# Kernel tuning notes

Measured on AMD Instinct MI355X. Metric: run time of the kernel, lower is better.

## Reference

```python
import jax, jax.numpy as jnp
import numpy as np

H1, H2 = 32, 16  # LSTM units per direction (layer 1, layer 2)
F = 64           # input feature dim


def lstm(x, W, U, b, reverse=False, return_sequences=True):
    """Keras-style LSTM. x: [B,T,F]. W:[F,4H], U:[H,4H], b:[4H].
    Gate order i,f,g,o; sigmoid recurrent activation, tanh activation.
    Dropout is inference-mode (identity). If reverse, process time backwards
    (go_backwards=True)."""
    if reverse:
        x = x[:, ::-1]
    B = x.shape[0]
    H = U.shape[0]
    xW = jnp.einsum('btf,fg->btg', x, W) + b  # [B,T,4H] precomputed input gates

    def step(carry, xw_t):
        h, c = carry
        z = xw_t + h @ U                       # [B,4H]
        i, f, g, o = jnp.split(z, 4, axis=-1)
        i = jax.nn.sigmoid(i)
        f = jax.nn.sigmoid(f)
        g = jnp.tanh(g)
        o = jax.nn.sigmoid(o)
        c = f * c + i * g
        h = o * jnp.tanh(c)
        return (h, c), h

    h0 = jnp.zeros((B, H), x.dtype)
    (h_last, _), hs = jax.lax.scan(step, (h0, h0), jnp.swapaxes(xW, 0, 1))
    if return_sequences:
        hs = jnp.swapaxes(hs, 0, 1)  # [B,T,H]
        if reverse:
            hs = hs[:, ::-1]  # Bidirectional re-reverses backward outputs
        return hs
    return h_last


def setup_inputs() -> dict:
    key = jax.random.key(0)
    ks = jax.random.split(key, 17)
    s = 0.05
    d = {
        'inputs': jax.random.normal(ks[0], (4096, 128, F), jnp.float32),
        # layer 1 (bidirectional, 32 units each dir)
        'W1f': jax.random.normal(ks[1], (F, 4 * H1)) * s,
        'U1f': jax.random.normal(ks[2], (H1, 4 * H1)) * s,
        'b1f': jnp.zeros((4 * H1,)),
        'W1b': jax.random.normal(ks[3], (F, 4 * H1)) * s,
        'U1b': jax.random.normal(ks[4], (H1, 4 * H1)) * s,
        'b1b': jnp.zeros((4 * H1,)),
        # layer 2 (bidirectional, 16 units each dir, input 2*H1=64)
        'W2f': jax.random.normal(ks[5], (2 * H1, 4 * H2)) * s,
        'U2f': jax.random.normal(ks[6], (H2, 4 * H2)) * s,
        'b2f': jnp.zeros((4 * H2,)),
        'W2b': jax.random.normal(ks[7], (2 * H1, 4 * H2)) * s,
        'U2b': jax.random.normal(ks[8], (H2, 4 * H2)) * s,
        'b2b': jnp.zeros((4 * H2,)),
        # dense head
        'W3': jax.random.normal(ks[9], (2 * H2, 8)) * s,
        'b3': jnp.zeros((8,)),
        'W4': jax.random.normal(ks[10], (8, 2)) * s,
        'b4': jnp.zeros((2,)),
    }
    return d


def reference(inputs, W1f, U1f, b1f, W1b, U1b, b1b,
              W2f, U2f, b2f, W2b, U2b, b2b, W3, b3, W4, b4):
    # bi_one: concat(forward seq, time-aligned backward seq) -> [B,T,64]
    h1f = lstm(inputs, W1f, U1f, b1f, reverse=False, return_sequences=True)
    h1b = lstm(inputs, W1b, U1b, b1b, reverse=True, return_sequences=True)
    x = jnp.concatenate([h1f, h1b], axis=-1)
    # bi_two: last hidden state of each direction -> [B,32]
    h2f = lstm(x, W2f, U2f, b2f, reverse=False, return_sequences=False)
    h2b = lstm(x, W2b, U2b, b2b, reverse=True, return_sequences=False)
    x = jnp.concatenate([h2f, h2b], axis=-1)
    x = x @ W3 + b3
    x = x * jax.nn.sigmoid(x)  # swish
    x = x @ W4 + b4
    return jax.nn.sigmoid(x)
```

## Files before the change

### kernel.cpp

```cpp
#include <hip/hip_runtime.h>
#include <hip/hip_bf16.h>

#define T 128
#define F 64
#define H1 32
#define G1 128
#define H2 16
#define G2 64

typedef __attribute__((ext_vector_type(8))) short bf16x8;
typedef __attribute__((ext_vector_type(4))) float f32x4;

__device__ __forceinline__ float sigmoidf_(float x) {
    return __builtin_amdgcn_rcpf(1.0f + __expf(-x));
}
__device__ __forceinline__ float tanhf_(float x) {
    return 1.0f - 2.0f * __builtin_amdgcn_rcpf(__expf(2.0f * x) + 1.0f);
}
__device__ __forceinline__ unsigned short f2bf(float f) {
    union { float f; unsigned u; } c; c.f = f;
    unsigned r = c.u + 0x7FFF + ((c.u >> 16) & 1);
    return (unsigned short)(r >> 16);
}
__device__ __forceinline__ void lds_barrier() {
    asm volatile("s_waitcnt lgkmcnt(0)" ::: "memory");
    __builtin_amdgcn_s_barrier();
}

__global__ __launch_bounds__(256) void xcvt(
    const float* __restrict__ x,
    unsigned short* __restrict__ xbf)
{
    __shared__ unsigned short tile[1024];
    const int g  = blockIdx.x;
    const int t0 = blockIdx.y * 8;
    const int m  = threadIdx.x >> 4;
    const int c4 = threadIdx.x & 15;
    const int ks   = c4 >> 3;
    const int quad = (c4 & 7) >> 1;
    const int j0   = (c4 & 1) * 4;
    const int slot = ks * 512 + (m + 16 * quad) * 8 + j0;

    for (int tt = 0; tt < 8; ++tt) {
        const int t = t0 + tt;
        const float4 v = *(const float4*)(x + ((size_t)(g * 16 + m) * T + t) * 64 + c4 * 4);
        ushort4 u;
        u.x = f2bf(v.x); u.y = f2bf(v.y); u.z = f2bf(v.z); u.w = f2bf(v.w);
        *(ushort4*)(tile + slot) = u;
        __syncthreads();
        *(uint2*)(xbf + (size_t)(g * T + t) * 1024 + threadIdx.x * 4) =
            *(const uint2*)(tile + threadIdx.x * 4);
        __syncthreads();
    }
}

__global__ __launch_bounds__(256, 2) void lstm1_fused(
    const unsigned short* __restrict__ xbf,
    const float* __restrict__ W1f, const float* __restrict__ b1f, const float* __restrict__ U1f,
    const float* __restrict__ W1b, const float* __restrict__ b1b, const float* __restrict__ U1b,
    unsigned short* __restrict__ h1)
{
    __shared__ unsigned short hb[2][16 * 40];
    const int tid  = threadIdx.x;
    const int lane = tid & 63;
    const int wv   = __builtin_amdgcn_readfirstlane(tid >> 6);
    const int gh   = wv & 1;
    const int sh   = wv >> 1;
    const int n15  = lane & 15, quad = lane >> 4;
    const int d    = blockIdx.x & 1, g = blockIdx.x >> 1;

    const float* W  = d ? W1b : W1f;
    const float* U  = d ? U1b : U1f;
    const float* bs = d ? b1b : b1f;

    bf16x8 Wf[4][2], Uf[4];
    f32x4 biasC[4];
    #pragma unroll
    for (int i = 0; i < 4; ++i) {
        const int col = (2 * i + gh) * 16 + n15;
        biasC[i] = (f32x4)(bs[col]);
        #pragma unroll
        for (int ks = 0; ks < 2; ++ks) {
            bf16x8 f;
            #pragma unroll
            for (int j = 0; j < 8; ++j)
                f[j] = (short)f2bf(W[(ks * 32 + quad * 8 + j) * G1 + col]);
            Wf[i][ks] = f;
        }
        bf16x8 u;
        #pragma unroll
        for (int j = 0; j < 8; ++j)
            u[j] = (short)f2bf(U[(quad * 8 + j) * G1 + col]);
        Uf[i] = u;
    }

    #pragma unroll
    for (int i = 0; i < 5; ++i) ((unsigned short*)hb)[tid + i * 256] = 0;

    float c0 = 0.0f, c1 = 0.0f;
    const unsigned short* xb = xbf + (size_t)g * T * 1024 + lane * 8;
    unsigned short* h1b0 = h1 + (size_t)g * T * 1024
        + d * 512 + ((quad * 4 + 2 * sh) + 16 * (gh * 2 + (n15 >> 3))) * 8 + (n15 & 7);
    unsigned short* h1b1 = h1b0 + 8;

    f32x4 xaA[4], xaB[4];
    bf16x8 xA0, xA1, xB0, xB1;
    {
        const unsigned short* p0 = xb + (size_t)(d ? (T - 1) : 0) * 1024;
        bf16x8 t0 = *(const bf16x8*)(p0), t1 = *(const bf16x8*)(p0 + 512);
        #pragma unroll
        for (int i = 0; i < 4; ++i) {
            xaA[i] = __builtin_amdgcn_mfma_f32_16x16x32_bf16(t0, Wf[i][0], biasC[i], 0, 0, 0);
            xaA[i] = __builtin_amdgcn_mfma_f32_16x16x32_bf16(t1, Wf[i][1], xaA[i], 0, 0, 0);
        }
        const unsigned short* p1 = xb + (size_t)(d ? (T - 2) : 1) * 1024;
        t0 = *(const bf16x8*)(p1); t1 = *(const bf16x8*)(p1 + 512);
        #pragma unroll
        for (int i = 0; i < 4; ++i) {
            xaB[i] = __builtin_amdgcn_mfma_f32_16x16x32_bf16(t0, Wf[i][0], biasC[i], 0, 0, 0);
            xaB[i] = __builtin_amdgcn_mfma_f32_16x16x32_bf16(t1, Wf[i][1], xaB[i], 0, 0, 0);
        }
        const unsigned short* p2 = xb + (size_t)(d ? (T - 3) : 2) * 1024;
        xA0 = *(const bf16x8*)(p2); xA1 = *(const bf16x8*)(p2 + 512);
        const unsigned short* p3 = xb + (size_t)(d ? (T - 4) : 3) * 1024;
        xB0 = *(const bf16x8*)(p3); xB1 = *(const bf16x8*)(p3 + 512);
    }
    lds_barrier();

    auto step = [&](int s, f32x4* xa, bf16x8& x0, bf16x8& x1) {
        const bf16x8 af = *(const bf16x8*)(hb[s & 1] + n15 * 40 + quad * 8);
        f32x4 a0 = __builtin_amdgcn_mfma_f32_16x16x32_bf16(af, Uf[0], xa[0], 0, 0, 0);
        f32x4 a1 = __builtin_amdgcn_mfma_f32_16x16x32_bf16(af, Uf[1], xa[1], 0, 0, 0);
        f32x4 a2 = __builtin_amdgcn_mfma_f32_16x16x32_bf16(af, Uf[2], xa[2], 0, 0, 0);
        f32x4 a3 = __builtin_amdgcn_mfma_f32_16x16x32_bf16(af, Uf[3], xa[3], 0, 0, 0);

        xa[0] = __builtin_amdgcn_mfma_f32_16x16x32_bf16(x0, Wf[0][0], biasC[0], 0, 0, 0);
        xa[1] = __builtin_amdgcn_mfma_f32_16x16x32_bf16(x0, Wf[1][0], biasC[1], 0, 0, 0);
        xa[2] = __builtin_amdgcn_mfma_f32_16x16x32_bf16(x0, Wf[2][0], biasC[2], 0, 0, 0);
        xa[3] = __builtin_amdgcn_mfma_f32_16x16x32_bf16(x0, Wf[3][0], biasC[3], 0, 0, 0);
        xa[0] = __builtin_amdgcn_mfma_f32_16x16x32_bf16(x1, Wf[0][1], xa[0], 0, 0, 0);
        xa[1] = __builtin_amdgcn_mfma_f32_16x16x32_bf16(x1, Wf[1][1], xa[1], 0, 0, 0);
        xa[2] = __builtin_amdgcn_mfma_f32_16x16x32_bf16(x1, Wf[2][1], xa[2], 0, 0, 0);
        xa[3] = __builtin_amdgcn_mfma_f32_16x16x32_bf16(x1, Wf[3][1], xa[3], 0, 0, 0);

        if (s + 4 < T) {
            const unsigned short* pn = xb + (size_t)(d ? (T - 5 - s) : (s + 4)) * 1024;
            x0 = *(const bf16x8*)(pn); x1 = *(const bf16x8*)(pn + 512);
        }

        const int t = d ? (T - 1 - s) : s;
        float zi0, zi1, zf0, zf1, zg0, zg1, zo0, zo1;
        if (sh == 0) {
            zi0 = a0[0]; zi1 = a0[1]; zf0 = a1[0]; zf1 = a1[1];
            zg0 = a2[0]; zg1 = a2[1]; zo0 = a3[0]; zo1 = a3[1];
        } else {
            zi0 = a0[2]; zi1 = a0[3]; zf0 = a1[2]; zf1 = a1[3];
            zg0 = a2[2]; zg1 = a2[3]; zo0 = a3[2]; zo1 = a3[3];
        }
        {
            const float ig = sigmoidf_(zi0);
            const float fg = sigmoidf_(zf0);
            const float gg = tanhf_(zg0);
            const float og = sigmoidf_(zo0);
            c0 = fg * c0 + ig * gg;
            const float h = og * tanhf_(c0);
            const unsigned short us = f2bf(h);
            hb[(s + 1) & 1][(quad * 4 + 2 * sh) * 40 + gh * 16 + n15] = us;
            h1b0[(size_t)t * 1024] = us;
        }
        {
            const float ig = sigmoidf_(zi1);
            const float fg = sigmoidf_(zf1);
            const float gg = tanhf_(zg1);
            const float og = sigmoidf_(zo1);
            c1 = fg * c1 + ig * gg;
            const float h = og * tanhf_(c1);
            const unsigned short us = f2bf(h);
            hb[(s + 1) & 1][(quad * 4 + 2 * sh + 1) * 40 + gh * 16 + n15] = us;
            h1b1[(size_t)t * 1024] = us;
        }
        lds_barrier();
    };

    #pragma unroll 1
    for (int s = 0; s < T; s += 2) {
        step(s, xaA, xA0, xA1);
        step(s + 1, xaB, xB0, xB1);
    }
}

__global__ __launch_bounds__(512, 2) void lstm2_head(
    const unsigned short* __restrict__ h1,
    const float* __restrict__ W2f, const float* __restrict__ b2f, const float* __restrict__ U2f,
    const float* __restrict__ W2b, const float* __restrict__ b2b, const float* __restrict__ U2b,
    const float* __restrict__ W3, const float* __restrict__ b3,
    const float* __restrict__ W4, const float* __restrict__ b4,
    float* __restrict__ out)
{
    __shared__ unsigned short hb2[2][2][400];
    __shared__ float hfin[2][16][16];
    __shared__ float ybuf[16][9];
    const int tid  = threadIdx.x;
    const int lane = tid & 63;
    const int wv   = __builtin_amdgcn_readfirstlane(tid >> 6);
    const int d    = wv & 1;
    const int sh   = wv >> 1;
    const int n15  = lane & 15, quad = lane >> 4;
    const int g    = blockIdx.x;

    const float* W  = d ? W2b : W2f;
    const float* U  = d ? U2b : U2f;
    const float* bs = d ? b2b : b2f;

    bf16x8 Wf[4][2], Uf[4];
    f32x4 biasC[4];
    #pragma unroll
    for (int i = 0; i < 4; ++i) {
        const int col = i * 16 + n15;
        biasC[i] = (f32x4)(bs[col]);
        #pragma unroll
        for (int ks = 0; ks < 2; ++ks) {
            bf16x8 f;
            #pragma unroll
            for (int j = 0; j < 8; ++j)
                f[j] = (short)f2bf(W[(ks * 32 + quad * 8 + j) * G2 + col]);
            Wf[i][ks] = f;
        }
        bf16x8 u;
        #pragma unroll
        for (int j = 0; j < 8; ++j) {
            const int k = quad * 8 + j;
            u[j] = (k < H2) ? (short)f2bf(U[k * G2 + col]) : (short)0;
        }
        Uf[i] = u;
    }

    #pragma unroll
    for (int i = 0; i < 4; ++i) {
        const int idx = tid + i * 512;
        if (idx < 1600) ((unsigned short*)hb2)[idx] = 0;
    }

    float c = 0.0f, hlast = 0.0f;
    const unsigned short* hl = h1 + (size_t)g * T * 1024 + lane * 8;

    f32x4 xaA[4], xaB[4];
    bf16x8 hA0, hA1, hB0, hB1;
    {
        const unsigned short* p0 = hl + (size_t)(d ? (T - 1) : 0) * 1024;
        bf16x8 t0 = *(const bf16x8*)(p0), t1 = *(const bf16x8*)(p0 + 512);
        #pragma unroll
        for (int i = 0; i < 4; ++i) {
            xaA[i] = __builtin_amdgcn_mfma_f32_16x16x32_bf16(t0, Wf[i][0], biasC[i], 0, 0, 0);
            xaA[i] = __builtin_amdgcn_mfma_f32_16x16x32_bf16(t1, Wf[i][1], xaA[i], 0, 0, 0);
        }
        const unsigned short* p1 = hl + (size_t)(d ? (T - 2) : 1) * 1024;
        t0 = *(const bf16x8*)(p1); t1 = *(const bf16x8*)(p1 + 512);
        #pragma unroll
        for (int i = 0; i < 4; ++i) {
            xaB[i] = __builtin_amdgcn_mfma_f32_16x16x32_bf16(t0, Wf[i][0], biasC[i], 0, 0, 0);
            xaB[i] = __builtin_amdgcn_mfma_f32_16x16x32_bf16(t1, Wf[i][1], xaB[i], 0, 0, 0);
        }
        const unsigned short* p2 = hl + (size_t)(d ? (T - 3) : 2) * 1024;
        hA0 = *(const bf16x8*)(p2); hA1 = *(const bf16x8*)(p2 + 512);
        const unsigned short* p3 = hl + (size_t)(d ? (T - 4) : 3) * 1024;
        hB0 = *(const bf16x8*)(p3); hB1 = *(const bf16x8*)(p3 + 512);
    }
    lds_barrier();

    auto step = [&](int s, f32x4* xa, bf16x8& x0, bf16x8& x1) {
        const bf16x8 af = *(const bf16x8*)(hb2[d][s & 1] + n15 * 24 + quad * 8);
        f32x4 a0 = __builtin_amdgcn_mfma_f32_16x16x32_bf16(af, Uf[0], xa[0], 0, 0, 0);
        f32x4 a1 = __builtin_amdgcn_mfma_f32_16x16x32_bf16(af, Uf[1], xa[1], 0, 0, 0);
        f32x4 a2 = __builtin_amdgcn_mfma_f32_16x16x32_bf16(af, Uf[2], xa[2], 0, 0, 0);
        f32x4 a3 = __builtin_amdgcn_mfma_f32_16x16x32_bf16(af, Uf[3], xa[3], 0, 0, 0);

        xa[0] = __builtin_amdgcn_mfma_f32_16x16x32_bf16(x0, Wf[0][0], biasC[0], 0, 0, 0);
        xa[1] = __builtin_amdgcn_mfma_f32_16x16x32_bf16(x0, Wf[1][0], biasC[1], 0, 0, 0);
        xa[2] = __builtin_amdgcn_mfma_f32_16x16x32_bf16(x0, Wf[2][0], biasC[2], 0, 0, 0);
        xa[3] = __builtin_amdgcn_mfma_f32_16x16x32_bf16(x0, Wf[3][0], biasC[3], 0, 0, 0);
        xa[0] = __builtin_amdgcn_mfma_f32_16x16x32_bf16(x1, Wf[0][1], xa[0], 0, 0, 0);
        xa[1] = __builtin_amdgcn_mfma_f32_16x16x32_bf16(x1, Wf[1][1], xa[1], 0, 0, 0);
        xa[2] = __builtin_amdgcn_mfma_f32_16x16x32_bf16(x1, Wf[2][1], xa[2], 0, 0, 0);
        xa[3] = __builtin_amdgcn_mfma_f32_16x16x32_bf16(x1, Wf[3][1], xa[3], 0, 0, 0);

        if (s + 4 < T) {
            const unsigned short* pn = hl + (size_t)(d ? (T - 5 - s) : (s + 4)) * 1024;
            x0 = *(const bf16x8*)(pn); x1 = *(const bf16x8*)(pn + 512);
        }

        float z0, z1, z2, z3;
        if (sh == 0)      { z0 = a0[0]; z1 = a1[0]; z2 = a2[0]; z3 = a3[0]; }
        else if (sh == 1) { z0 = a0[1]; z1 = a1[1]; z2 = a2[1]; z3 = a3[1]; }
        else if (sh == 2) { z0 = a0[2]; z1 = a1[2]; z2 = a2[2]; z3 = a3[2]; }
        else              { z0 = a0[3]; z1 = a1[3]; z2 = a2[3]; z3 = a3[3]; }
        const float ig = sigmoidf_(z0);
        const float fg = sigmoidf_(z1);
        const float gg = tanhf_(z2);
        const float og = sigmoidf_(z3);
        c = fg * c + ig * gg;
        hlast = og * tanhf_(c);
        hb2[d][(s + 1) & 1][(quad * 4 + sh) * 24 + n15] = f2bf(hlast);
        lds_barrier();
    };

    #pragma unroll 1
    for (int s = 0; s < T; s += 2) {
        step(s, xaA, hA0, hA1);
        step(s + 1, xaB, hB0, hB1);
    }

    hfin[d][quad * 4 + sh][n15] = hlast;
    __syncthreads();

    if (tid < 128) {
        const int s = tid >> 3, u = tid & 7;
        float a = b3[u];
        #pragma unroll
        for (int k = 0; k < H2; ++k) a += hfin[0][s][k] * W3[k * 8 + u];
        #pragma unroll
        for (int k = 0; k < H2; ++k) a += hfin[1][s][k] * W3[(H2 + k) * 8 + u];
        ybuf[s][u] = a * sigmoidf_(a);
    }
    __syncthreads();
    if (tid < 32) {
        const int s = tid >> 1, o = tid & 1;
        float a = b4[o];
        #pragma unroll
        for (int k = 0; k < 8; ++k) a += ybuf[s][k] * W4[k * 2 + o];
        out[(size_t)(g * 16 + s) * 2 + o] = sigmoidf_(a);
    }
}

extern "C" void kernel_launch(void* const* d_in, const int* in_sizes, int n_in,
                              void* d_out, int out_size, void* d_ws, size_t ws_size,
                              hipStream_t stream) {
    const float* x   = (const float*)d_in[0];
    const float* W1f = (const float*)d_in[1];
    const float* U1f = (const float*)d_in[2];
    const float* b1f = (const float*)d_in[3];
    const float* W1b = (const float*)d_in[4];
    const float* U1b = (const float*)d_in[5];
    const float* b1b = (const float*)d_in[6];
    const float* W2f = (const float*)d_in[7];
    const float* U2f = (const float*)d_in[8];
    const float* b2f = (const float*)d_in[9];
    const float* W2b = (const float*)d_in[10];
    const float* U2b = (const float*)d_in[11];
    const float* b2b = (const float*)d_in[12];
    const float* W3  = (const float*)d_in[13];
    const float* b3  = (const float*)d_in[14];
    const float* W4  = (const float*)d_in[15];
    const float* b4  = (const float*)d_in[16];
    float* out = (float*)d_out;

    const int B  = in_sizes[0] / (T * F);
    const int NG = B / 16;

    const size_t perG = (size_t)T * 1024 * sizeof(unsigned short);
    int chG = (int)(ws_size / (2 * perG));
    if (chG > NG) chG = NG;
    if (chG < 1) chG = 1;
    unsigned short* xbf = (unsigned short*)d_ws;
    unsigned short* h1  = xbf + (size_t)chG * T * 1024;

    for (int g0 = 0; g0 < NG; g0 += chG) {
        const int cg = (NG - g0 < chG) ? (NG - g0) : chG;
        dim3 gcv(cg, T / 8);
        xcvt<<<gcv, 256, 0, stream>>>(x + (size_t)g0 * 16 * T * F, xbf);
        lstm1_fused<<<cg * 2, 256, 0, stream>>>(
            xbf, W1f, b1f, U1f, W1b, b1b, U1b, h1);
        lstm2_head<<<cg, 512, 0, stream>>>(
            h1, W2f, b2f, U2f, W2b, b2b, U2b, W3, b3, W4, b4,
            out + (size_t)g0 * 16 * 2);
    }
}
```

Baseline: 383.4 us.

## Split layer-2 LSTM per direction, separate dense head, simplify input conversion

Layer-2 now runs one direction per 256-thread block instead of both directions in one 512-thread block. This doubles the block count and is meant to improve occupancy and parallelism on the serial recurrence. The dense head moves into its own small kernel, which reads final hidden states stored in the xbf workspace. The input bf16 conversion becomes a one-float4-per-thread scatter with no LDS staging or barriers, at the cost of less coalesced stores and one extra kernel launch per chunk.

```diff
diff --git a/kernel.cpp b/kernel.cpp
--- a/kernel.cpp
+++ b/kernel.cpp
@@ -11,6 +11,8 @@
 typedef __attribute__((ext_vector_type(8))) short bf16x8;
 typedef __attribute__((ext_vector_type(4))) float f32x4;
 
+#define MFMA __builtin_amdgcn_mfma_f32_16x16x32_bf16
+
 __device__ __forceinline__ float sigmoidf_(float x) {
     return __builtin_amdgcn_rcpf(1.0f + __expf(-x));
 }
@@ -31,27 +33,21 @@
     const float* __restrict__ x,
     unsigned short* __restrict__ xbf)
 {
-    __shared__ unsigned short tile[1024];
-    const int g  = blockIdx.x;
-    const int t0 = blockIdx.y * 8;
-    const int m  = threadIdx.x >> 4;
-    const int c4 = threadIdx.x & 15;
-    const int ks   = c4 >> 3;
-    const int quad = (c4 & 7) >> 1;
-    const int j0   = (c4 & 1) * 4;
-    const int slot = ks * 512 + (m + 16 * quad) * 8 + j0;
-
-    for (int tt = 0; tt < 8; ++tt) {
-        const int t = t0 + tt;
-        const float4 v = *(const float4*)(x + ((size_t)(g * 16 + m) * T + t) * 64 + c4 * 4);
-        ushort4 u;
-        u.x = f2bf(v.x); u.y = f2bf(v.y); u.z = f2bf(v.z); u.w = f2bf(v.w);
-        *(ushort4*)(tile + slot) = u;
-        __syncthreads();
-        *(uint2*)(xbf + (size_t)(g * T + t) * 1024 + threadIdx.x * 4) =
-            *(const uint2*)(tile + threadIdx.x * 4);
-        __syncthreads();
-    }
+    const size_t fi = (size_t)blockIdx.x * 256 + threadIdx.x;
+    const int c4 = (int)(fi & 15);
+    const size_t row = fi >> 4;
+    const int t = (int)(row & (T - 1));
+    const size_t b = row >> 7;
+    const int m = (int)(b & 15);
+    const size_t g = b >> 4;
+
+    const float4 v = *(const float4*)(x + fi * 4);
+    ushort4 u;
+    u.x = f2bf(v.x); u.y = f2bf(v.y); u.z = f2bf(v.z); u.w = f2bf(v.w);
+    const int ks = c4 >> 3;
+    const int q  = (c4 & 7) >> 1;
+    const int j0 = (c4 & 1) * 4;
+    *(ushort4*)(xbf + ((size_t)(g * T + t)) * 1024 + ks * 512 + (m + 16 * q) * 8 + j0) = u;
 }
 
 __global__ __launch_bounds__(256, 2) void lstm1_fused(
@@ -110,15 +106,15 @@
         bf16x8 t0 = *(const bf16x8*)(p0), t1 = *(const bf16x8*)(p0 + 512);
         #pragma unroll
         for (int i = 0; i < 4; ++i) {
-            xaA[i] = __builtin_amdgcn_mfma_f32_16x16x32_bf16(t0, Wf[i][0], biasC[i], 0, 0, 0);
-            xaA[i] = __builtin_amdgcn_mfma_f32_16x16x32_bf16(t1, Wf[i][1], xaA[i], 0, 0, 0);
+            xaA[i] = MFMA(t0, Wf[i][0], biasC[i], 0, 0, 0);
+            xaA[i] = MFMA(t1, Wf[i][1], xaA[i], 0, 0, 0);
         }
         const unsigned short* p1 = xb + (size_t)(d ? (T - 2) : 1) * 1024;
         t0 = *(const bf16x8*)(p1); t1 = *(const bf16x8*)(p1 + 512);
         #pragma unroll
         for (int i = 0; i < 4; ++i) {
-            xaB[i] = __builtin_amdgcn_mfma_f32_16x16x32_bf16(t0, Wf[i][0], biasC[i], 0, 0, 0);
-            xaB[i] = __builtin_amdgcn_mfma_f32_16x16x32_bf16(t1, Wf[i][1], xaB[i], 0, 0, 0);
+            xaB[i] = MFMA(t0, Wf[i][0], biasC[i], 0, 0, 0);
+            xaB[i] = MFMA(t1, Wf[i][1], xaB[i], 0, 0, 0);
         }
         const unsigned short* p2 = xb + (size_t)(d ? (T - 3) : 2) * 1024;
         xA0 = *(const bf16x8*)(p2); xA1 = *(const bf16x8*)(p2 + 512);
@@ -129,19 +125,19 @@
 
     auto step = [&](int s, f32x4* xa, bf16x8& x0, bf16x8& x1) {
         const bf16x8 af = *(const bf16x8*)(hb[s & 1] + n15 * 40 + quad * 8);
-        f32x4 a0 = __builtin_amdgcn_mfma_f32_16x16x32_bf16(af, Uf[0], xa[0], 0, 0, 0);
-        f32x4 a1 = __builtin_amdgcn_mfma_f32_16x16x32_bf16(af, Uf[1], xa[1], 0, 0, 0);
-        f32x4 a2 = __builtin_amdgcn_mfma_f32_16x16x32_bf16(af, Uf[2], xa[2], 0, 0, 0);
-        f32x4 a3 = __builtin_amdgcn_mfma_f32_16x16x32_bf16(af, Uf[3], xa[3], 0, 0, 0);
-
-        xa[0] = __builtin_amdgcn_mfma_f32_16x16x32_bf16(x0, Wf[0][0], biasC[0], 0, 0, 0);
-        xa[1] = __builtin_amdgcn_mfma_f32_16x16x32_bf16(x0, Wf[1][0], biasC[1], 0, 0, 0);
-        xa[2] = __builtin_amdgcn_mfma_f32_16x16x32_bf16(x0, Wf[2][0], biasC[2], 0, 0, 0);
-        xa[3] = __builtin_amdgcn_mfma_f32_16x16x32_bf16(x0, Wf[3][0], biasC[3], 0, 0, 0);
-        xa[0] = __builtin_amdgcn_mfma_f32_16x16x32_bf16(x1, Wf[0][1], xa[0], 0, 0, 0);
-        xa[1] = __builtin_amdgcn_mfma_f32_16x16x32_bf16(x1, Wf[1][1], xa[1], 0, 0, 0);
-        xa[2] = __builtin_amdgcn_mfma_f32_16x16x32_bf16(x1, Wf[2][1], xa[2], 0, 0, 0);
-        xa[3] = __builtin_amdgcn_mfma_f32_16x16x32_bf16(x1, Wf[3][1], xa[3], 0, 0, 0);
+        f32x4 a0 = MFMA(af, Uf[0], xa[0], 0, 0, 0);
+        f32x4 a1 = MFMA(af, Uf[1], xa[1], 0, 0, 0);
+        f32x4 a2 = MFMA(af, Uf[2], xa[2], 0, 0, 0);
+        f32x4 a3 = MFMA(af, Uf[3], xa[3], 0, 0, 0);
+
+        xa[0] = MFMA(x0, Wf[0][0], biasC[0], 0, 0, 0);
+        xa[1] = MFMA(x0, Wf[1][0], biasC[1], 0, 0, 0);
+        xa[2] = MFMA(x0, Wf[2][0], biasC[2], 0, 0, 0);
+        xa[3] = MFMA(x0, Wf[3][0], biasC[3], 0, 0, 0);
+        xa[0] = MFMA(x1, Wf[0][1], xa[0], 0, 0, 0);
+        xa[1] = MFMA(x1, Wf[1][1], xa[1], 0, 0, 0);
+        xa[2] = MFMA(x1, Wf[2][1], xa[2], 0, 0, 0);
+        xa[3] = MFMA(x1, Wf[3][1], xa[3], 0, 0, 0);
 
         if (s + 4 < T) {
             const unsigned short* pn = xb + (size_t)(d ? (T - 5 - s) : (s + 4)) * 1024;
@@ -158,10 +154,8 @@
             zg0 = a2[2]; zg1 = a2[3]; zo0 = a3[2]; zo1 = a3[3];
         }
         {
-            const float ig = sigmoidf_(zi0);
-            const float fg = sigmoidf_(zf0);
-            const float gg = tanhf_(zg0);
-            const float og = sigmoidf_(zo0);
+            const float ig = sigmoidf_(zi0), fg = sigmoidf_(zf0);
+            const float gg = tanhf_(zg0),   og = sigmoidf_(zo0);
             c0 = fg * c0 + ig * gg;
             const float h = og * tanhf_(c0);
             const unsigned short us = f2bf(h);
@@ -169,10 +163,8 @@
             h1b0[(size_t)t * 1024] = us;
         }
         {
-            const float ig = sigmoidf_(zi1);
-            const float fg = sigmoidf_(zf1);
-            const float gg = tanhf_(zg1);
-            const float og = sigmoidf_(zo1);
+            const float ig = sigmoidf_(zi1), fg = sigmoidf_(zf1);
+            const float gg = tanhf_(zg1),   og = sigmoidf_(zo1);
             c1 = fg * c1 + ig * gg;
             const float h = og * tanhf_(c1);
             const unsigned short us = f2bf(h);
@@ -189,24 +181,18 @@
     }
 }
 
-__global__ __launch_bounds__(512, 2) void lstm2_head(
+__global__ __launch_bounds__(256, 2) void lstm2_rec(
     const unsigned short* __restrict__ h1,
     const float* __restrict__ W2f, const float* __restrict__ b2f, const float* __restrict__ U2f,
     const float* __restrict__ W2b, const float* __restrict__ b2b, const float* __restrict__ U2b,
-    const float* __restrict__ W3, const float* __restrict__ b3,
-    const float* __restrict__ W4, const float* __restrict__ b4,
-    float* __restrict__ out)
+    float* __restrict__ hfin)
 {
-    __shared__ unsigned short hb2[2][2][400];
-    __shared__ float hfin[2][16][16];
-    __shared__ float ybuf[16][9];
+    __shared__ unsigned short hx[2][16 * 40];
     const int tid  = threadIdx.x;
     const int lane = tid & 63;
-    const int wv   = __builtin_amdgcn_readfirstlane(tid >> 6);
-    const int d    = wv & 1;
-    const int sh   = wv >> 1;
+    const int sh   = __builtin_amdgcn_readfirstlane(tid >> 6);
     const int n15  = lane & 15, quad = lane >> 4;
-    const int g    = blockIdx.x;
+    const int d    = blockIdx.x & 1, g = blockIdx.x >> 1;
 
     const float* W  = d ? W2b : W2f;
     const float* U  = d ? U2b : U2f;
@@ -226,20 +212,17 @@
                 f[j] = (short)f2bf(W[(ks * 32 + quad * 8 + j) * G2 + col]);
             Wf[i][ks] = f;
         }
-        bf16x8 u;
+        bf16x8 uu;
         #pragma unroll
         for (int j = 0; j < 8; ++j) {
             const int k = quad * 8 + j;
-            u[j] = (k < H2) ? (short)f2bf(U[k * G2 + col]) : (short)0;
-        }
-        Uf[i] = u;
-    }
-
-    #pragma unroll
-    for (int i = 0; i < 4; ++i) {
-        const int idx = tid + i * 512;
-        if (idx < 1600) ((unsigned short*)hb2)[idx] = 0;
-    }
+            uu[j] = (k < H2) ? (short)f2bf(U[k * G2 + col]) : (short)0;
+        }
+        Uf[i] = uu;
+    }
+
+    #pragma unroll
+    for (int i = 0; i < 5; ++i) ((unsigned short*)hx)[tid + i * 256] = 0;
 
     float c = 0.0f, hlast = 0.0f;
     const unsigned short* hl = h1 + (size_t)g * T * 1024 + lane * 8;
@@ -251,15 +234,15 @@
         bf16x8 t0 = *(const bf16x8*)(p0), t1 = *(const bf16x8*)(p0 + 512);
         #pragma unroll
         for (int i = 0; i < 4; ++i) {
-            xaA[i] = __builtin_amdgcn_mfma_f32_16x16x32_bf16(t0, Wf[i][0], biasC[i], 0, 0, 0);
-            xaA[i] = __builtin_amdgcn_mfma_f32_16x16x32_bf16(t1, Wf[i][1], xaA[i], 0, 0, 0);
+            xaA[i] = MFMA(t0, Wf[i][0], biasC[i], 0, 0, 0);
+            xaA[i] = MFMA(t1, Wf[i][1], xaA[i], 0, 0, 0);
         }
         const unsigned short* p1 = hl + (size_t)(d ? (T - 2) : 1) * 1024;
         t0 = *(const bf16x8*)(p1); t1 = *(const bf16x8*)(p1 + 512);
         #pragma unroll
         for (int i = 0; i < 4; ++i) {
-            xaB[i] = __builtin_amdgcn_mfma_f32_16x16x32_bf16(t0, Wf[i][0], biasC[i], 0, 0, 0);
-            xaB[i] = __builtin_amdgcn_mfma_f32_16x16x32_bf16(t1, Wf[i][1], xaB[i], 0, 0, 0);
+            xaB[i] = MFMA(t0, Wf[i][0], biasC[i], 0, 0, 0);
+            xaB[i] = MFMA(t1, Wf[i][1], xaB[i], 0, 0, 0);
         }
         const unsigned short* p2 = hl + (size_t)(d ? (T - 3) : 2) * 1024;
         hA0 = *(const bf16x8*)(p2); hA1 = *(const bf16x8*)(p2 + 512);
@@ -269,20 +252,20 @@
     lds_barrier();
 
     auto step = [&](int s, f32x4* xa, bf16x8& x0, bf16x8& x1) {
-        const bf16x8 af = *(const bf16x8*)(hb2[d][s & 1] + n15 * 24 + quad * 8);
-        f32x4 a0 = __builtin_amdgcn_mfma_f32_16x16x32_bf16(af, Uf[0], xa[0], 0, 0, 0);
-        f32x4 a1 = __builtin_amdgcn_mfma_f32_16x16x32_bf16(af, Uf[1], xa[1], 0, 0, 0);
-        f32x4 a2 = __builtin_amdgcn_mfma_f32_16x16x32_bf16(af, Uf[2], xa[2], 0, 0, 0);
-        f32x4 a3 = __builtin_amdgcn_mfma_f32_16x16x32_bf16(af, Uf[3], xa[3], 0, 0, 0);
-
-        xa[0] = __builtin_amdgcn_mfma_f32_16x16x32_bf16(x0, Wf[0][0], biasC[0], 0, 0, 0);
-        xa[1] = __builtin_amdgcn_mfma_f32_16x16x32_bf16(x0, Wf[1][0], biasC[1], 0, 0, 0);
-        xa[2] = __builtin_amdgcn_mfma_f32_16x16x32_bf16(x0, Wf[2][0], biasC[2], 0, 0, 0);
-        xa[3] = __builtin_amdgcn_mfma_f32_16x16x32_bf16(x0, Wf[3][0], biasC[3], 0, 0, 0);
-        xa[0] = __builtin_amdgcn_mfma_f32_16x16x32_bf16(x1, Wf[0][1], xa[0], 0, 0, 0);
-        xa[1] = __builtin_amdgcn_mfma_f32_16x16x32_bf16(x1, Wf[1][1], xa[1], 0, 0, 0);
-        xa[2] = __builtin_amdgcn_mfma_f32_16x16x32_bf16(x1, Wf[2][1], xa[2], 0, 0, 0);
-        xa[3] = __builtin_amdgcn_mfma_f32_16x16x32_bf16(x1, Wf[3][1], xa[3], 0, 0, 0);
+        const bf16x8 af = *(const bf16x8*)(hx[s & 1] + n15 * 40 + quad * 8);
+        f32x4 a0 = MFMA(af, Uf[0], xa[0], 0, 0, 0);
+        f32x4 a1 = MFMA(af, Uf[1], xa[1], 0, 0, 0);
+        f32x4 a2 = MFMA(af, Uf[2], xa[2], 0, 0, 0);
+        f32x4 a3 = MFMA(af, Uf[3], xa[3], 0, 0, 0);
+
+        xa[0] = MFMA(x0, Wf[0][0], biasC[0], 0, 0, 0);
+        xa[1] = MFMA(x0, Wf[1][0], biasC[1], 0, 0, 0);
+        xa[2] = MFMA(x0, Wf[2][0], biasC[2], 0, 0, 0);
+        xa[3] = MFMA(x0, Wf[3][0], biasC[3], 0, 0, 0);
+        xa[0] = MFMA(x1, Wf[0][1], xa[0], 0, 0, 0);
+        xa[1] = MFMA(x1, Wf[1][1], xa[1], 0, 0, 0);
+        xa[2] = MFMA(x1, Wf[2][1], xa[2], 0, 0, 0);
+        xa[3] = MFMA(x1, Wf[3][1], xa[3], 0, 0, 0);
 
         if (s + 4 < T) {
             const unsigned short* pn = hl + (size_t)(d ? (T - 5 - s) : (s + 4)) * 1024;
@@ -294,13 +277,11 @@
         else if (sh == 1) { z0 = a0[1]; z1 = a1[1]; z2 = a2[1]; z3 = a3[1]; }
         else if (sh == 2) { z0 = a0[2]; z1 = a1[2]; z2 = a2[2]; z3 = a3[2]; }
         else              { z0 = a0[3]; z1 = a1[3]; z2 = a2[3]; z3 = a3[3]; }
-        const float ig = sigmoidf_(z0);
-        const float fg = sigmoidf_(z1);
-        const float gg = tanhf_(z2);
-        const float og = sigmoidf_(z3);
+        const float ig = sigmoidf_(z0), fg = sigmoidf_(z1);
+        const float gg = tanhf_(z2),   og = sigmoidf_(z3);
         c = fg * c + ig * gg;
         hlast = og * tanhf_(c);
-        hb2[d][(s + 1) & 1][(quad * 4 + sh) * 24 + n15] = f2bf(hlast);
+        hx[(s + 1) & 1][(quad * 4 + sh) * 40 + n15] = f2bf(hlast);
         lds_barrier();
     };
 
@@ -310,25 +291,35 @@
         step(s + 1, xaB, hB0, hB1);
     }
 
-    hfin[d][quad * 4 + sh][n15] = hlast;
-    __syncthreads();
-
-    if (tid < 128) {
-        const int s = tid >> 3, u = tid & 7;
+    hfin[(size_t)(g * 16 + quad * 4 + sh) * 32 + d * 16 + n15] = hlast;
+}
+
+__global__ __launch_bounds__(256) void head(
+    const float* __restrict__ hfin,
+    const float* __restrict__ W3, const float* __restrict__ b3,
+    const float* __restrict__ W4, const float* __restrict__ b4,
+    float* __restrict__ out, const int ns)
+{
+    const int i = blockIdx.x * 256 + threadIdx.x;
+    if (i >= ns) return;
+    float h[32];
+    #pragma unroll
+    for (int k = 0; k < 8; ++k)
+        *(float4*)(h + k * 4) = *(const float4*)(hfin + (size_t)i * 32 + k * 4);
+    float y[8];
+    #pragma unroll
+    for (int u = 0; u < 8; ++u) {
         float a = b3[u];
         #pragma unroll
-        for (int k = 0; k < H2; ++k) a += hfin[0][s][k] * W3[k * 8 + u];
-        #pragma unroll
-        for (int k = 0; k < H2; ++k) a += hfin[1][s][k] * W3[(H2 + k) * 8 + u];
-        ybuf[s][u] = a * sigmoidf_(a);
-    }
-    __syncthreads();
-    if (tid < 32) {
-        const int s = tid >> 1, o = tid & 1;
+        for (int k = 0; k < 32; ++k) a += h[k] * W3[k * 8 + u];
+        y[u] = a * sigmoidf_(a);
+    }
+    #pragma unroll
+    for (int o = 0; o < 2; ++o) {
         float a = b4[o];
         #pragma unroll
-        for (int k = 0; k < 8; ++k) a += ybuf[s][k] * W4[k * 2 + o];
-        out[(size_t)(g * 16 + s) * 2 + o] = sigmoidf_(a);
+        for (int u = 0; u < 8; ++u) a += y[u] * W4[u * 2 + o];
+        out[(size_t)i * 2 + o] = sigmoidf_(a);
     }
 }
 
@@ -366,12 +357,13 @@
 
     for (int g0 = 0; g0 < NG; g0 += chG) {
         const int cg = (NG - g0 < chG) ? (NG - g0) : chG;
-        dim3 gcv(cg, T / 8);
-        xcvt<<<gcv, 256, 0, stream>>>(x + (size_t)g0 * 16 * T * F, xbf);
+        const int nf4 = cg * 16 * T * 16;
+        xcvt<<<nf4 / 256, 256, 0, stream>>>(x + (size_t)g0 * 16 * T * F, xbf);
         lstm1_fused<<<cg * 2, 256, 0, stream>>>(
             xbf, W1f, b1f, U1f, W1b, b1b, U1b, h1);
-        lstm2_head<<<cg, 512, 0, stream>>>(
-            h1, W2f, b2f, U2f, W2b, b2b, U2b, W3, b3, W4, b4,
-            out + (size_t)g0 * 16 * 2);
-    }
-}
+        lstm2_rec<<<cg * 2, 256, 0, stream>>>(
+            h1, W2f, b2f, U2f, W2b, b2b, U2b, (float*)xbf);
+        head<<<(cg * 16 + 255) / 256, 256, 0, stream>>>(
+            (float*)xbf, W3, b3, W4, b4, out + (size_t)g0 * 16 * 2, cg * 16);
+    }
+}
```

After: 369.8 us. 3.6% less time.
